# Optimization experiments

Measured on AMD Instinct MI355X. Metric: run time of the kernel, lower is better.

The kernel has to match this reference:

```python
import jax, jax.numpy as jnp
import numpy as np

N = 50000          # nodes
E = 800000         # edges (before self-loops)
IN_CH = 128
HID = 64
HEADS = 4
NEG_SLOPE = 0.2    # PyG GATConv default negative_slope


def _gat_conv(x, W, a_src, a_dst, bias, src, dst, heads, out_ch):
    """PyG-style GATConv (concat=True). src/dst already include self-loops."""
    n = x.shape[0]
    h = (x @ W).reshape(n, heads, out_ch)                 # [N,H,C]
    # per-node attention halves: a_src . h_i  and  a_dst . h_i
    es = (h * a_src[None]).sum(-1)                        # [N,H]
    ed = (h * a_dst[None]).sum(-1)                        # [N,H]
    logits = jax.nn.leaky_relu(es[src] + ed[dst], NEG_SLOPE)   # [Etot,H]
    # segment softmax over incoming edges of each dst node
    m = jax.ops.segment_max(logits, dst, num_segments=n)       # [N,H]
    m = jnp.where(jnp.isfinite(m), m, jnp.zeros_like(m))
    p = jnp.exp(logits - m[dst])                               # [Etot,H]
    s = jax.ops.segment_sum(p, dst, num_segments=n)            # [N,H]
    att = p / (s[dst] + 1e-16)                                 # [Etot,H]
    msg = h[src] * att[..., None]                              # [Etot,H,C]
    out = jax.ops.segment_sum(msg, dst, num_segments=n)        # [N,H,C]
    return out.reshape(n, heads * out_ch) + bias


def setup_inputs() -> dict:
    key = jax.random.key(0)
    ks = jax.random.split(key, 12)
    x = jax.random.normal(ks[0], (N, IN_CH), dtype=jnp.float32)
    edge_index = jax.random.randint(ks[1], (2, E), 0, N, dtype=jnp.int32)
    def glorot(k, shape, fan_in):
        return jax.random.normal(k, shape, dtype=jnp.float32) * (1.0 / np.sqrt(fan_in))
    return {
        "x": x,
        "W1": glorot(ks[2], (IN_CH, HEADS * HID), IN_CH),
        "a_src1": glorot(ks[3], (HEADS, HID), HID),
        "a_dst1": glorot(ks[4], (HEADS, HID), HID),
        "b1": jnp.zeros((HEADS * HID,), dtype=jnp.float32),
        "W2": glorot(ks[5], (HEADS * HID, HID), HEADS * HID),
        "a_src2": glorot(ks[6], (1, HID), HID),
        "a_dst2": glorot(ks[7], (1, HID), HID),
        "b2": jnp.zeros((HID,), dtype=jnp.float32),
        "Wo": glorot(ks[8], (HID, 1), HID),
        "bo": jnp.zeros((1,), dtype=jnp.float32),
        "edge_index": edge_index,
    }


def reference(x, W1, a_src1, a_dst1, b1, W2, a_src2, a_dst2, b2, Wo, bo, edge_index):
    n = x.shape[0]
    loops = jnp.arange(n, dtype=edge_index.dtype)          # add_self_loops=True (PyG default)
    src = jnp.concatenate([edge_index[0], loops])
    dst = jnp.concatenate([edge_index[1], loops])
    h = jax.nn.elu(_gat_conv(x, W1, a_src1, a_dst1, b1, src, dst, HEADS, HID))
    # dropout inactive in eval mode
    h = jax.nn.elu(_gat_conv(h, W2, a_src2, a_dst2, b2, src, dst, 1, HID))
    return (h @ Wo + bo).squeeze(-1)                       # [N]
```

## Files before the change

kernel.cpp:

```cpp
#include <hip/hip_runtime.h>
#include <cmath>

#define LRELU_SLOPE 0.2f

static inline int cdiv_h(int a, int b){ return (a + b - 1) / b; }

__device__ __forceinline__ float dev_lrelu(float x){ return x > 0.f ? x : LRELU_SLOPE * x; }
__device__ __forceinline__ float dev_elu(float x){ return x > 0.f ? x : expm1f(x); }

__device__ __forceinline__ unsigned short f2bf(float f){
  unsigned int u = __float_as_uint(f);
  u = (u + 0x7FFFu + ((u >> 16) & 1u)) >> 16;
  return (unsigned short)u;
}
__device__ __forceinline__ float bf2f_lo(unsigned int u){
  return __uint_as_float(u << 16);
}
__device__ __forceinline__ float bf2f_hi(unsigned int u){
  return __uint_as_float(u & 0xFFFF0000u);
}

__device__ __forceinline__ float edge_w(float logit){
  return __expf(fminf(logit, 80.f));
}

typedef __attribute__((ext_vector_type(8))) short bf16x8;
typedef __attribute__((ext_vector_type(4))) float f32x4;

#define CNT_STRIDE 16

__global__ void prep_kernel(const float* __restrict__ W1, unsigned short* __restrict__ W1T,
                            const float* __restrict__ W2, unsigned short* __restrict__ W2T,
                            int* __restrict__ cnt, int n)
{
  int b = blockIdx.x, t = threadIdx.x;
  if (b < 128){
    int i = b * 256 + t;
    int k = i >> 8, c = i & 255;
    W1T[(size_t)c * 128 + k] = f2bf(W1[i]);
  } else if (b < 192){
    int i = (b - 128) * 256 + t;
    int k = i >> 6, c = i & 63;
    W2T[(size_t)c * 256 + k] = f2bf(W2[i]);
  } else {
    int i = (b - 192) * 256 + t;
    if (i < n) cnt[(size_t)i * CNT_STRIDE] = 1;
  }
}


__global__ void scan_blocks_kernel(const int* __restrict__ cnt, int* __restrict__ rowptr,
                                   int n, int* __restrict__ bsum){
  __shared__ int sd[256];
  int idx = blockIdx.x * 256 + threadIdx.x;
  int v = (idx < n) ? cnt[(size_t)idx * CNT_STRIDE] : 0;
  sd[threadIdx.x] = v;
  __syncthreads();
  #pragma unroll
  for (int off = 1; off < 256; off <<= 1){
    int x = (threadIdx.x >= off) ? sd[threadIdx.x - off] : 0;
    __syncthreads();
    sd[threadIdx.x] += x;
    __syncthreads();
  }
  if (idx < n) rowptr[idx] = sd[threadIdx.x] - v;
  if (threadIdx.x == 255) bsum[blockIdx.x] = sd[255];
}

__global__ void scan_add_kernel(int* __restrict__ rowptr, int n, const int* __restrict__ bsum,
                                int total, unsigned short* __restrict__ col){
  __shared__ int red[256];
  int t = threadIdx.x;
  int p = 0;
  for (int k = t; k < (int)blockIdx.x; k += 256) p += bsum[k];
  red[t] = p;
  __syncthreads();
  #pragma unroll
  for (int off = 128; off > 0; off >>= 1){
    if (t < off) red[t] += red[t + off];
    __syncthreads();
  }
  int prefix = red[0];
  int idx = blockIdx.x * 256 + t;
  if (idx < n){
    int v = rowptr[idx] + prefix;
    rowptr[idx] = v;
    col[v] = (unsigned short)idx;
  }
  if (idx == 0) rowptr[n] = total;
}

__global__ void scatter_kernel(const int* __restrict__ ei, const int* __restrict__ rank,
                               const int* __restrict__ rowptr, int e, unsigned short* __restrict__ col){
  int i = blockIdx.x * blockDim.x + threadIdx.x;
  if (i >= e) return;
  int s = ei[i], d = ei[e + i];
  col[rowptr[d] + rank[i]] = (unsigned short)s;
}

__launch_bounds__(256)
__global__ void gemm1_mfma_kernel(const float* __restrict__ A, const unsigned short* __restrict__ BT,
                                  unsigned short* __restrict__ Cb,
                                  const float* __restrict__ a_src, const float* __restrict__ a_dst,
                                  float* __restrict__ es, float* __restrict__ ed,
                                  int M, int K, int GB,
                                  const int* __restrict__ hist_dst, int He,
                                  int* __restrict__ cnt, int* __restrict__ rank)
{
  constexpr int BN = 256, NSUB = 16, H = 4;
  constexpr int LDK = 40;
  __shared__ short As[64 * LDK];
  __shared__ short Bs[BN * LDK];
  const int tid = threadIdx.x;

  if (blockIdx.x >= GB){
    int i = (blockIdx.x - GB) * 256 + tid;
    if (i < He){
      int d = hist_dst[i];
      rank[i] = atomicAdd(&cnt[(size_t)d * CNT_STRIDE], 1);
    }
    return;
  }

  const int bm = blockIdx.x;
  const int wave = tid >> 6, lane = tid & 63;
  const int lm = lane & 15, quad = lane >> 4;
  const int arow = tid >> 2, kc8 = (tid & 3) * 8;
  const int gm_a = bm * 64 + arow;

  f32x4 acc[NSUB];
  #pragma unroll
  for (int i = 0; i < NSUB; i++) acc[i] = (f32x4){0.f, 0.f, 0.f, 0.f};

  for (int k0 = 0; k0 < K; k0 += 32){
    unsigned short a8[8];
    float4 t0 = {0,0,0,0}, t1 = {0,0,0,0};
    if (gm_a < M){
      t0 = *(const float4*)&A[(size_t)gm_a * K + k0 + kc8];
      t1 = *(const float4*)&A[(size_t)gm_a * K + k0 + kc8 + 4];
    }
    a8[0] = f2bf(t0.x); a8[1] = f2bf(t0.y); a8[2] = f2bf(t0.z); a8[3] = f2bf(t0.w);
    a8[4] = f2bf(t1.x); a8[5] = f2bf(t1.y); a8[6] = f2bf(t1.z); a8[7] = f2bf(t1.w);
    uint4 b8[4];
    #pragma unroll
    for (int rep = 0; rep < 4; rep++){
      int brow = rep * 64 + arow;
      b8[rep] = *(const uint4*)&BT[(size_t)brow * K + k0 + kc8];
    }
    __syncthreads();
    *(uint4*)&As[arow * LDK + kc8] = *(uint4*)a8;
    #pragma unroll
    for (int rep = 0; rep < 4; rep++)
      *(uint4*)&Bs[(rep * 64 + arow) * LDK + kc8] = b8[rep];
    __syncthreads();
    bf16x8 af = *(const bf16x8*)&As[(wave * 16 + lm) * LDK + quad * 8];
    #pragma unroll
    for (int nb = 0; nb < NSUB; nb++){
      bf16x8 bfr = *(const bf16x8*)&Bs[(nb * 16 + lm) * LDK + quad * 8];
      acc[nb] = __builtin_amdgcn_mfma_f32_16x16x32_bf16(af, bfr, acc[nb], 0, 0, 0);
    }
  }

  float asv[NSUB], adv[NSUB];
  #pragma unroll
  for (int nb = 0; nb < NSUB; nb++){
    asv[nb] = a_src[nb * 16 + lm];
    adv[nb] = a_dst[nb * 16 + lm];
  }
  #pragma unroll
  for (int r = 0; r < 4; r++){
    int gm = bm * 64 + wave * 16 + quad * 4 + r;
    if (gm < M){
      #pragma unroll
      for (int nb = 0; nb < NSUB; nb++)
        Cb[(size_t)gm * BN + nb * 16 + lm] = f2bf(acc[nb][r]);
    }
    #pragma unroll
    for (int h = 0; h < H; h++){
      float ps = 0.f, pd = 0.f;
      #pragma unroll
      for (int nbh = 0; nbh < 4; nbh++){
        int nb = h * 4 + nbh;
        float a = acc[nb][r];
        ps += a * asv[nb];
        pd += a * adv[nb];
      }
      #pragma unroll
      for (int off = 1; off < 16; off <<= 1){
        ps += __shfl_xor(ps, off, 64);
        pd += __shfl_xor(pd, off, 64);
      }
      if (lm == 0 && gm < M){
        es[(size_t)gm * H + h] = ps;
        ed[(size_t)gm * H + h] = pd;
      }
    }
  }
}

__launch_bounds__(256)
__global__ void gemm2_mfma_kernel(const unsigned short* __restrict__ A, const unsigned short* __restrict__ BT,
                                  unsigned short* __restrict__ Cb,
                                  const float* __restrict__ a_src, const float* __restrict__ a_dst,
                                  float* __restrict__ es, float* __restrict__ ed,
                                  int M, int K)
{
  constexpr int BN = 64, NSUB = 4;
  constexpr int LDK = 40;
  __shared__ short As[128 * LDK];
  __shared__ short Bs[64 * LDK];
  const int tid = threadIdx.x;
  const int bm = blockIdx.x;
  const int wave = tid >> 6, lane = tid & 63;
  const int lm = lane & 15, quad = lane >> 4;
  const int arow = tid >> 2, kc8 = (tid & 3) * 8;
  const int gm_a0 = bm * 128 + arow;
  const int gm_a1 = gm_a0 + 64;

  f32x4 acc0[NSUB], acc1[NSUB];
  #pragma unroll
  for (int i = 0; i < NSUB; i++){
    acc0[i] = (f32x4){0.f, 0.f, 0.f, 0.f};
    acc1[i] = (f32x4){0.f, 0.f, 0.f, 0.f};
  }

  for (int k0 = 0; k0 < K; k0 += 32){
    uint4 a0 = make_uint4(0,0,0,0), a1 = make_uint4(0,0,0,0);
    if (gm_a0 < M) a0 = *(const uint4*)&A[(size_t)gm_a0 * K + k0 + kc8];
    if (gm_a1 < M) a1 = *(const uint4*)&A[(size_t)gm_a1 * K + k0 + kc8];
    uint4 b = *(const uint4*)&BT[(size_t)arow * K + k0 + kc8];
    __syncthreads();
    *(uint4*)&As[arow * LDK + kc8] = a0;
    *(uint4*)&As[(64 + arow) * LDK + kc8] = a1;
    *(uint4*)&Bs[arow * LDK + kc8] = b;
    __syncthreads();
    bf16x8 af0 = *(const bf16x8*)&As[(wave * 16 + lm) * LDK + quad * 8];
    bf16x8 af1 = *(const bf16x8*)&As[(64 + wave * 16 + lm) * LDK + quad * 8];
    #pragma unroll
    for (int nb = 0; nb < NSUB; nb++){
      bf16x8 bfr = *(const bf16x8*)&Bs[(nb * 16 + lm) * LDK + quad * 8];
      acc0[nb] = __builtin_amdgcn_mfma_f32_16x16x32_bf16(af0, bfr, acc0[nb], 0, 0, 0);
      acc1[nb] = __builtin_amdgcn_mfma_f32_16x16x32_bf16(af1, bfr, acc1[nb], 0, 0, 0);
    }
  }

  float asv[NSUB], adv[NSUB];
  #pragma unroll
  for (int nb = 0; nb < NSUB; nb++){
    asv[nb] = a_src[nb * 16 + lm];
    adv[nb] = a_dst[nb * 16 + lm];
  }
  #pragma unroll
  for (int half = 0; half < 2; half++){
    #pragma unroll
    for (int r = 0; r < 4; r++){
      int gm = bm * 128 + half * 64 + wave * 16 + quad * 4 + r;
      float ps = 0.f, pd = 0.f;
      #pragma unroll
      for (int nb = 0; nb < NSUB; nb++){
        float a = half ? acc1[nb][r] : acc0[nb][r];
        if (gm < M) Cb[(size_t)gm * BN + nb * 16 + lm] = f2bf(a);
        ps += a * asv[nb];
        pd += a * adv[nb];
      }
      #pragma unroll
      for (int off = 1; off < 16; off <<= 1){
        ps += __shfl_xor(ps, off, 64);
        pd += __shfl_xor(pd, off, 64);
      }
      if (lm == 0 && gm < M){
        es[gm] = ps;
        ed[gm] = pd;
      }
    }
  }
}

__global__ void agg1_kernel(const unsigned short* __restrict__ h1b, const float* __restrict__ es,
                            const float* __restrict__ ed,
                            const int* __restrict__ rowptr, const unsigned short* __restrict__ col,
                            const float* __restrict__ b1, unsigned short* __restrict__ out1b, int n)
{
  int node = blockIdx.x * 8 + (threadIdx.x >> 5);
  if (node >= n) return;
  int r = threadIdx.x & 31;
  int h = r >> 3;
  float edh = ed[node * 4 + h];
  int start = rowptr[node], end = rowptr[node + 1];
  float l = 0.f;
  float a0=0.f,a1=0.f,a2=0.f,a3=0.f,a4=0.f,a5=0.f,a6=0.f,a7=0.f;
  int j = start;
  for (; j + 3 < end; j += 4){
    int s0 = col[j], s1 = col[j+1], s2 = col[j+2], s3 = col[j+3];
    float e0 = es[s0*4 + h], e1 = es[s1*4 + h], e2 = es[s2*4 + h], e3 = es[s3*4 + h];
    uint4 r0 = *(const uint4*)&h1b[(size_t)s0 * 256 + r * 8];
    uint4 r1 = *(const uint4*)&h1b[(size_t)s1 * 256 + r * 8];
    uint4 r2 = *(const uint4*)&h1b[(size_t)s2 * 256 + r * 8];
    uint4 r3 = *(const uint4*)&h1b[(size_t)s3 * 256 + r * 8];
    float w0 = edge_w(dev_lrelu(e0 + edh));
    float w1 = edge_w(dev_lrelu(e1 + edh));
    float w2 = edge_w(dev_lrelu(e2 + edh));
    float w3 = edge_w(dev_lrelu(e3 + edh));
    l += w0 + w1 + w2 + w3;
    a0 += bf2f_lo(r0.x)*w0 + bf2f_lo(r1.x)*w1 + bf2f_lo(r2.x)*w2 + bf2f_lo(r3.x)*w3;
    a1 += bf2f_hi(r0.x)*w0 + bf2f_hi(r1.x)*w1 + bf2f_hi(r2.x)*w2 + bf2f_hi(r3.x)*w3;
    a2 += bf2f_lo(r0.y)*w0 + bf2f_lo(r1.y)*w1 + bf2f_lo(r2.y)*w2 + bf2f_lo(r3.y)*w3;
    a3 += bf2f_hi(r0.y)*w0 + bf2f_hi(r1.y)*w1 + bf2f_hi(r2.y)*w2 + bf2f_hi(r3.y)*w3;
    a4 += bf2f_lo(r0.z)*w0 + bf2f_lo(r1.z)*w1 + bf2f_lo(r2.z)*w2 + bf2f_lo(r3.z)*w3;
    a5 += bf2f_hi(r0.z)*w0 + bf2f_hi(r1.z)*w1 + bf2f_hi(r2.z)*w2 + bf2f_hi(r3.z)*w3;
    a6 += bf2f_lo(r0.w)*w0 + bf2f_lo(r1.w)*w1 + bf2f_lo(r2.w)*w2 + bf2f_lo(r3.w)*w3;
    a7 += bf2f_hi(r0.w)*w0 + bf2f_hi(r1.w)*w1 + bf2f_hi(r2.w)*w2 + bf2f_hi(r3.w)*w3;
  }
  for (; j < end; j++){
    int s0 = col[j];
    float w0 = edge_w(dev_lrelu(es[s0*4 + h] + edh));
    uint4 r0 = *(const uint4*)&h1b[(size_t)s0 * 256 + r * 8];
    l += w0;
    a0 += bf2f_lo(r0.x)*w0; a1 += bf2f_hi(r0.x)*w0;
    a2 += bf2f_lo(r0.y)*w0; a3 += bf2f_hi(r0.y)*w0;
    a4 += bf2f_lo(r0.z)*w0; a5 += bf2f_hi(r0.z)*w0;
    a6 += bf2f_lo(r0.w)*w0; a7 += bf2f_hi(r0.w)*w0;
  }
  float inv = 1.f / l;
  float4 bA = *(const float4*)&b1[r * 8];
  float4 bB = *(const float4*)&b1[r * 8 + 4];
  uint4 o;
  o.x = (unsigned int)f2bf(dev_elu(a0*inv + bA.x)) | ((unsigned int)f2bf(dev_elu(a1*inv + bA.y)) << 16);
  o.y = (unsigned int)f2bf(dev_elu(a2*inv + bA.z)) | ((unsigned int)f2bf(dev_elu(a3*inv + bA.w)) << 16);
  o.z = (unsigned int)f2bf(dev_elu(a4*inv + bB.x)) | ((unsigned int)f2bf(dev_elu(a5*inv + bB.y)) << 16);
  o.w = (unsigned int)f2bf(dev_elu(a6*inv + bB.z)) | ((unsigned int)f2bf(dev_elu(a7*inv + bB.w)) << 16);
  *(uint4*)&out1b[(size_t)node * 256 + r * 8] = o;
}

__global__ void agg2_kernel(const unsigned short* __restrict__ h2b, const float* __restrict__ es,
                            const float* __restrict__ ed,
                            const int* __restrict__ rowptr, const unsigned short* __restrict__ col,
                            const float* __restrict__ b2, const float* __restrict__ Wo,
                            const float* __restrict__ bo, float* __restrict__ out, int n)
{
  int node = blockIdx.x * 16 + (threadIdx.x >> 4);
  if (node >= n) return;
  int r = threadIdx.x & 15;
  float edh = ed[node];
  int start = rowptr[node], end = rowptr[node + 1];
  float l = 0.f;
  float a0=0.f,a1=0.f,a2=0.f,a3=0.f;
  int j = start;
  for (; j + 3 < end; j += 4){
    int s0 = col[j], s1 = col[j+1], s2 = col[j+2], s3 = col[j+3];
    float e0 = es[s0], e1 = es[s1], e2 = es[s2], e3 = es[s3];
    uint2 r0 = *(const uint2*)&h2b[(size_t)s0 * 64 + r * 4];
    uint2 r1 = *(const uint2*)&h2b[(size_t)s1 * 64 + r * 4];
    uint2 r2 = *(const uint2*)&h2b[(size_t)s2 * 64 + r * 4];
    uint2 r3 = *(const uint2*)&h2b[(size_t)s3 * 64 + r * 4];
    float w0 = edge_w(dev_lrelu(e0 + edh));
    float w1 = edge_w(dev_lrelu(e1 + edh));
    float w2 = edge_w(dev_lrelu(e2 + edh));
    float w3 = edge_w(dev_lrelu(e3 + edh));
    l += w0 + w1 + w2 + w3;
    a0 += bf2f_lo(r0.x)*w0 + bf2f_lo(r1.x)*w1 + bf2f_lo(r2.x)*w2 + bf2f_lo(r3.x)*w3;
    a1 += bf2f_hi(r0.x)*w0 + bf2f_hi(r1.x)*w1 + bf2f_hi(r2.x)*w2 + bf2f_hi(r3.x)*w3;
    a2 += bf2f_lo(r0.y)*w0 + bf2f_lo(r1.y)*w1 + bf2f_lo(r2.y)*w2 + bf2f_lo(r3.y)*w3;
    a3 += bf2f_hi(r0.y)*w0 + bf2f_hi(r1.y)*w1 + bf2f_hi(r2.y)*w2 + bf2f_hi(r3.y)*w3;
  }
  for (; j < end; j++){
    int s0 = col[j];
    float w0 = edge_w(dev_lrelu(es[s0] + edh));
    uint2 r0 = *(const uint2*)&h2b[(size_t)s0 * 64 + r * 4];
    l += w0;
    a0 += bf2f_lo(r0.x)*w0; a1 += bf2f_hi(r0.x)*w0;
    a2 += bf2f_lo(r0.y)*w0; a3 += bf2f_hi(r0.y)*w0;
  }
  float inv = 1.f / l;
  float4 bb = *(const float4*)&b2[r * 4];
  float4 wo = *(const float4*)&Wo[r * 4];
  float t = dev_elu(a0*inv + bb.x) * wo.x
          + dev_elu(a1*inv + bb.y) * wo.y
          + dev_elu(a2*inv + bb.z) * wo.z
          + dev_elu(a3*inv + bb.w) * wo.w;
  #pragma unroll
  for (int off = 1; off < 16; off <<= 1) t += __shfl_xor(t, off, 64);
  if (r == 0) out[node] = t + bo[0];
}

extern "C" void kernel_launch(void* const* d_in, const int* in_sizes, int n_in,
                              void* d_out, int out_size, void* d_ws, size_t ws_size,
                              hipStream_t stream)
{
  const float* x    = (const float*)d_in[0];
  const float* W1   = (const float*)d_in[1];
  const float* a_s1 = (const float*)d_in[2];
  const float* a_d1 = (const float*)d_in[3];
  const float* b1   = (const float*)d_in[4];
  const float* W2   = (const float*)d_in[5];
  const float* a_s2 = (const float*)d_in[6];
  const float* a_d2 = (const float*)d_in[7];
  const float* b2   = (const float*)d_in[8];
  const float* Wo   = (const float*)d_in[9];
  const float* bo   = (const float*)d_in[10];
  const int*   ei   = (const int*)d_in[11];

  const int Nn = in_sizes[0] / 128;
  const int E  = in_sizes[11] / 2;
  const int ET = E + Nn;

  size_t off = 0;
  auto carve = [&](size_t bytes) -> void* {
    void* p = (char*)d_ws + off;
    off += (bytes + 255) & ~(size_t)255;
    return p;
  };
  unsigned short* h1b   = (unsigned short*)carve((size_t)Nn * 256 * sizeof(unsigned short));
  unsigned short* out1b = (unsigned short*)carve((size_t)Nn * 256 * sizeof(unsigned short));
  unsigned short* h2b   = (unsigned short*)carve((size_t)Nn * 64 * sizeof(unsigned short));
  unsigned short* W1T   = (unsigned short*)carve((size_t)128 * 256 * sizeof(unsigned short));
  unsigned short* W2T   = (unsigned short*)carve((size_t)256 * 64 * sizeof(unsigned short));
  float* es1    = (float*)carve((size_t)Nn * 4 * sizeof(float));
  float* ed1    = (float*)carve((size_t)Nn * 4 * sizeof(float));
  float* es2    = (float*)carve((size_t)Nn * sizeof(float));
  float* ed2    = (float*)carve((size_t)Nn * sizeof(float));
  int*   cnt    = (int*)carve((size_t)Nn * CNT_STRIDE * sizeof(int));
  int*   rowptr = (int*)carve((size_t)(Nn + 1) * sizeof(int));
  int*   rank   = (int*)carve((size_t)E * sizeof(int));
  int*   bsum   = (int*)carve(256 * sizeof(int));
  unsigned short* col = (unsigned short*)carve((size_t)ET * sizeof(unsigned short));
  float* out = (float*)d_out;

  int deg_blocks = cdiv_h(Nn, 256);
  prep_kernel<<<192 + deg_blocks, 256, 0, stream>>>(W1, W1T, W2, W2T, cnt, Nn);

  int GB1 = cdiv_h(Nn, 64);
  int HB  = cdiv_h(E, 256);
  gemm1_mfma_kernel<<<GB1 + HB, 256, 0, stream>>>(
      x, W1T, h1b, a_s1, a_d1, es1, ed1, Nn, 128, GB1, ei + E, E, cnt, rank);

  int nb = cdiv_h(Nn, 256);
  scan_blocks_kernel<<<nb, 256, 0, stream>>>(cnt, rowptr, Nn, bsum);
  scan_add_kernel<<<nb, 256, 0, stream>>>(rowptr, Nn, bsum, ET, col);
  scatter_kernel<<<cdiv_h(E, 256), 256, 0, stream>>>(ei, rank, rowptr, E, col);

  agg1_kernel<<<cdiv_h(Nn, 8), 256, 0, stream>>>(h1b, es1, ed1, rowptr, col, b1, out1b, Nn);

  gemm2_mfma_kernel<<<cdiv_h(Nn, 128), 256, 0, stream>>>(
      out1b, W2T, h2b, a_s2, a_d2, es2, ed2, Nn, 256);
  agg2_kernel<<<cdiv_h(Nn, 16), 256, 0, stream>>>(h2b, es2, ed2, rowptr, col, b2, Wo, bo, out, Nn);
}
```

Baseline: 254.0 us.

## Split each node's edge list across a full wavefront in both aggregation kernels

Both aggregation kernels now assign one 64-lane wavefront per destination node instead of 32 or 16 lanes. Lane groups take disjoint subsets of the incoming edges and combine partial sums with cross-lane shuffles. Column indices for the next iteration are also loaded one step ahead. The aim is more memory-level parallelism and shorter per-node serial loops for the gather-heavy aggregation. The cost is extra shuffle reductions, more blocks, and idle half-waves for low-degree nodes.

```diff
diff --git a/kernel.cpp b/kernel.cpp
--- a/kernel.cpp
+++ b/kernel.cpp
@@ -276,22 +276,44 @@
   }
 }
 
+#define AGG1_EDGE(jj) { \
+    int s0_ = col[jj]; \
+    float w0_ = edge_w(dev_lrelu(es[s0_*4 + h] + edh)); \
+    uint4 r0_ = *(const uint4*)&h1b[(size_t)s0_ * 256 + r * 8]; \
+    l += w0_; \
+    a0 += bf2f_lo(r0_.x)*w0_; a1 += bf2f_hi(r0_.x)*w0_; \
+    a2 += bf2f_lo(r0_.y)*w0_; a3 += bf2f_hi(r0_.y)*w0_; \
+    a4 += bf2f_lo(r0_.z)*w0_; a5 += bf2f_hi(r0_.z)*w0_; \
+    a6 += bf2f_lo(r0_.w)*w0_; a7 += bf2f_hi(r0_.w)*w0_; }
+
 __global__ void agg1_kernel(const unsigned short* __restrict__ h1b, const float* __restrict__ es,
                             const float* __restrict__ ed,
                             const int* __restrict__ rowptr, const unsigned short* __restrict__ col,
                             const float* __restrict__ b1, unsigned short* __restrict__ out1b, int n)
 {
-  int node = blockIdx.x * 8 + (threadIdx.x >> 5);
+  int node = blockIdx.x * 4 + (threadIdx.x >> 6);
   if (node >= n) return;
-  int r = threadIdx.x & 31;
+  int lane = threadIdx.x & 63;
+  int half = lane >> 5;
+  int r = lane & 31;
   int h = r >> 3;
   float edh = ed[node * 4 + h];
   int start = rowptr[node], end = rowptr[node + 1];
   float l = 0.f;
   float a0=0.f,a1=0.f,a2=0.f,a3=0.f,a4=0.f,a5=0.f,a6=0.f,a7=0.f;
   int j = start;
-  for (; j + 3 < end; j += 4){
-    int s0 = col[j], s1 = col[j+1], s2 = col[j+2], s3 = col[j+3];
+
+  int c0=0,c1=0,c2=0,c3=0;
+  if (j + 7 < end){
+    int b = j + half * 4;
+    c0 = col[b]; c1 = col[b+1]; c2 = col[b+2]; c3 = col[b+3];
+  }
+  for (; j + 7 < end; j += 8){
+    int s0 = c0, s1 = c1, s2 = c2, s3 = c3;
+    if (j + 15 < end){
+      int b = j + 8 + half * 4;
+      c0 = col[b]; c1 = col[b+1]; c2 = col[b+2]; c3 = col[b+3];
+    }
     float e0 = es[s0*4 + h], e1 = es[s1*4 + h], e2 = es[s2*4 + h], e3 = es[s3*4 + h];
     uint4 r0 = *(const uint4*)&h1b[(size_t)s0 * 256 + r * 8];
     uint4 r1 = *(const uint4*)&h1b[(size_t)s1 * 256 + r * 8];
@@ -311,26 +333,42 @@
     a6 += bf2f_lo(r0.w)*w0 + bf2f_lo(r1.w)*w1 + bf2f_lo(r2.w)*w2 + bf2f_lo(r3.w)*w3;
     a7 += bf2f_hi(r0.w)*w0 + bf2f_hi(r1.w)*w1 + bf2f_hi(r2.w)*w2 + bf2f_hi(r3.w)*w3;
   }
-  for (; j < end; j++){
-    int s0 = col[j];
-    float w0 = edge_w(dev_lrelu(es[s0*4 + h] + edh));
-    uint4 r0 = *(const uint4*)&h1b[(size_t)s0 * 256 + r * 8];
-    l += w0;
-    a0 += bf2f_lo(r0.x)*w0; a1 += bf2f_hi(r0.x)*w0;
-    a2 += bf2f_lo(r0.y)*w0; a3 += bf2f_hi(r0.y)*w0;
-    a4 += bf2f_lo(r0.z)*w0; a5 += bf2f_hi(r0.z)*w0;
-    a6 += bf2f_lo(r0.w)*w0; a7 += bf2f_hi(r0.w)*w0;
-  }
-  float inv = 1.f / l;
-  float4 bA = *(const float4*)&b1[r * 8];
-  float4 bB = *(const float4*)&b1[r * 8 + 4];
-  uint4 o;
-  o.x = (unsigned int)f2bf(dev_elu(a0*inv + bA.x)) | ((unsigned int)f2bf(dev_elu(a1*inv + bA.y)) << 16);
-  o.y = (unsigned int)f2bf(dev_elu(a2*inv + bA.z)) | ((unsigned int)f2bf(dev_elu(a3*inv + bA.w)) << 16);
-  o.z = (unsigned int)f2bf(dev_elu(a4*inv + bB.x)) | ((unsigned int)f2bf(dev_elu(a5*inv + bB.y)) << 16);
-  o.w = (unsigned int)f2bf(dev_elu(a6*inv + bB.z)) | ((unsigned int)f2bf(dev_elu(a7*inv + bB.w)) << 16);
-  *(uint4*)&out1b[(size_t)node * 256 + r * 8] = o;
-}
+  for (; j + 3 < end; j += 4){
+    int b = j + half * 2;
+    AGG1_EDGE(b); AGG1_EDGE(b + 1);
+  }
+  for (; j + 1 < end; j += 2){
+    AGG1_EDGE(j + half);
+  }
+  if (j < end && half == 0){
+    AGG1_EDGE(j);
+  }
+  l  += __shfl_xor(l , 32, 64);
+  a0 += __shfl_xor(a0, 32, 64);  a1 += __shfl_xor(a1, 32, 64);
+  a2 += __shfl_xor(a2, 32, 64);  a3 += __shfl_xor(a3, 32, 64);
+  a4 += __shfl_xor(a4, 32, 64);  a5 += __shfl_xor(a5, 32, 64);
+  a6 += __shfl_xor(a6, 32, 64);  a7 += __shfl_xor(a7, 32, 64);
+
+  if (half == 0){
+    float inv = 1.f / l;
+    float4 bA = *(const float4*)&b1[r * 8];
+    float4 bB = *(const float4*)&b1[r * 8 + 4];
+    uint4 o;
+    o.x = (unsigned int)f2bf(dev_elu(a0*inv + bA.x)) | ((unsigned int)f2bf(dev_elu(a1*inv + bA.y)) << 16);
+    o.y = (unsigned int)f2bf(dev_elu(a2*inv + bA.z)) | ((unsigned int)f2bf(dev_elu(a3*inv + bA.w)) << 16);
+    o.z = (unsigned int)f2bf(dev_elu(a4*inv + bB.x)) | ((unsigned int)f2bf(dev_elu(a5*inv + bB.y)) << 16);
+    o.w = (unsigned int)f2bf(dev_elu(a6*inv + bB.z)) | ((unsigned int)f2bf(dev_elu(a7*inv + bB.w)) << 16);
+    *(uint4*)&out1b[(size_t)node * 256 + r * 8] = o;
+  }
+}
+
+#define AGG2_EDGE(jj) { \
+    int s0_ = col[jj]; \
+    float w0_ = edge_w(dev_lrelu(es[s0_] + edh)); \
+    uint2 r0_ = *(const uint2*)&h2b[(size_t)s0_ * 64 + r * 4]; \
+    l += w0_; \
+    a0 += bf2f_lo(r0_.x)*w0_; a1 += bf2f_hi(r0_.x)*w0_; \
+    a2 += bf2f_lo(r0_.y)*w0_; a3 += bf2f_hi(r0_.y)*w0_; }
 
 __global__ void agg2_kernel(const unsigned short* __restrict__ h2b, const float* __restrict__ es,
                             const float* __restrict__ ed,
@@ -338,39 +376,54 @@
                             const float* __restrict__ b2, const float* __restrict__ Wo,
                             const float* __restrict__ bo, float* __restrict__ out, int n)
 {
-  int node = blockIdx.x * 16 + (threadIdx.x >> 4);
+  int node = blockIdx.x * 4 + (threadIdx.x >> 6);
   if (node >= n) return;
-  int r = threadIdx.x & 15;
+  int lane = threadIdx.x & 63;
+  int slot = lane >> 4;
+  int r = lane & 15;
   float edh = ed[node];
   int start = rowptr[node], end = rowptr[node + 1];
   float l = 0.f;
   float a0=0.f,a1=0.f,a2=0.f,a3=0.f;
   int j = start;
-  for (; j + 3 < end; j += 4){
-    int s0 = col[j], s1 = col[j+1], s2 = col[j+2], s3 = col[j+3];
-    float e0 = es[s0], e1 = es[s1], e2 = es[s2], e3 = es[s3];
+
+  int c0=0, c1=0;
+  if (j + 7 < end){
+    int b = j + slot * 2;
+    c0 = col[b]; c1 = col[b+1];
+  }
+  for (; j + 7 < end; j += 8){
+    int s0 = c0, s1 = c1;
+    if (j + 15 < end){
+      int b = j + 8 + slot * 2;
+      c0 = col[b]; c1 = col[b+1];
+    }
+    float e0 = es[s0], e1 = es[s1];
     uint2 r0 = *(const uint2*)&h2b[(size_t)s0 * 64 + r * 4];
     uint2 r1 = *(const uint2*)&h2b[(size_t)s1 * 64 + r * 4];
-    uint2 r2 = *(const uint2*)&h2b[(size_t)s2 * 64 + r * 4];
-    uint2 r3 = *(const uint2*)&h2b[(size_t)s3 * 64 + r * 4];
     float w0 = edge_w(dev_lrelu(e0 + edh));
     float w1 = edge_w(dev_lrelu(e1 + edh));
-    float w2 = edge_w(dev_lrelu(e2 + edh));
-    float w3 = edge_w(dev_lrelu(e3 + edh));
-    l += w0 + w1 + w2 + w3;
-    a0 += bf2f_lo(r0.x)*w0 + bf2f_lo(r1.x)*w1 + bf2f_lo(r2.x)*w2 + bf2f_lo(r3.x)*w3;
-    a1 += bf2f_hi(r0.x)*w0 + bf2f_hi(r1.x)*w1 + bf2f_hi(r2.x)*w2 + bf2f_hi(r3.x)*w3;
-    a2 += bf2f_lo(r0.y)*w0 + bf2f_lo(r1.y)*w1 + bf2f_lo(r2.y)*w2 + bf2f_lo(r3.y)*w3;
-    a3 += bf2f_hi(r0.y)*w0 + bf2f_hi(r1.y)*w1 + bf2f_hi(r2.y)*w2 + bf2f_hi(r3.y)*w3;
-  }
-  for (; j < end; j++){
-    int s0 = col[j];
-    float w0 = edge_w(dev_lrelu(es[s0] + edh));
-    uint2 r0 = *(const uint2*)&h2b[(size_t)s0 * 64 + r * 4];
-    l += w0;
-    a0 += bf2f_lo(r0.x)*w0; a1 += bf2f_hi(r0.x)*w0;
-    a2 += bf2f_lo(r0.y)*w0; a3 += bf2f_hi(r0.y)*w0;
-  }
+    l += w0 + w1;
+    a0 += bf2f_lo(r0.x)*w0 + bf2f_lo(r1.x)*w1;
+    a1 += bf2f_hi(r0.x)*w0 + bf2f_hi(r1.x)*w1;
+    a2 += bf2f_lo(r0.y)*w0 + bf2f_lo(r1.y)*w1;
+    a3 += bf2f_hi(r0.y)*w0 + bf2f_hi(r1.y)*w1;
+  }
+  for (; j + 3 < end; j += 4){
+    AGG2_EDGE(j + slot);
+  }
+  {
+    int rem = end - j;
+    if (slot < rem){
+      AGG2_EDGE(j + slot);
+    }
+  }
+  l  += __shfl_xor(l , 16, 64);  l  += __shfl_xor(l , 32, 64);
+  a0 += __shfl_xor(a0, 16, 64);  a0 += __shfl_xor(a0, 32, 64);
+  a1 += __shfl_xor(a1, 16, 64);  a1 += __shfl_xor(a1, 32, 64);
+  a2 += __shfl_xor(a2, 16, 64);  a2 += __shfl_xor(a2, 32, 64);
+  a3 += __shfl_xor(a3, 16, 64);  a3 += __shfl_xor(a3, 32, 64);
+
   float inv = 1.f / l;
   float4 bb = *(const float4*)&b2[r * 4];
   float4 wo = *(const float4*)&Wo[r * 4];
@@ -380,7 +433,7 @@
           + dev_elu(a3*inv + bb.w) * wo.w;
   #pragma unroll
   for (int off = 1; off < 16; off <<= 1) t += __shfl_xor(t, off, 64);
-  if (r == 0) out[node] = t + bo[0];
+  if (lane == 0) out[node] = t + bo[0];
 }
 
 extern "C" void kernel_launch(void* const* d_in, const int* in_sizes, int n_in,
@@ -439,9 +492,9 @@
   scan_add_kernel<<<nb, 256, 0, stream>>>(rowptr, Nn, bsum, ET, col);
   scatter_kernel<<<cdiv_h(E, 256), 256, 0, stream>>>(ei, rank, rowptr, E, col);
 
-  agg1_kernel<<<cdiv_h(Nn, 8), 256, 0, stream>>>(h1b, es1, ed1, rowptr, col, b1, out1b, Nn);
+  agg1_kernel<<<cdiv_h(Nn, 4), 256, 0, stream>>>(h1b, es1, ed1, rowptr, col, b1, out1b, Nn);
 
   gemm2_mfma_kernel<<<cdiv_h(Nn, 128), 256, 0, stream>>>(
       out1b, W2T, h2b, a_s2, a_d2, es2, ed2, Nn, 256);
-  agg2_kernel<<<cdiv_h(Nn, 16), 256, 0, stream>>>(h2b, es2, ed2, rowptr, col, b2, Wo, bo, out, Nn);
-}
+  agg2_kernel<<<cdiv_h(Nn, 4), 256, 0, stream>>>(h2b, es2, ed2, rowptr, col, b2, Wo, bo, out, Nn);
+}
```

Result: slower. 260.4 us (+2.5%).

## Fuse layer-1 aggregation with layer-2 GEMM and split edges across half-waves

Applied to the files above, without the earlier changes.

Merges the layer-1 attention aggregation and the layer-2 projection GEMM into one kernel. Each block aggregates 4 nodes into shared memory, then one wave runs MFMA against W2T, read straight from global memory, to produce h2 and the attention logits. This removes the out1b round trip through global memory and one kernel launch. Each node now gets a full wave instead of half a wave, with the two half-waves splitting the edges and prefetching the next column indices. In exchange, only one wave per block does the GEMM, 12 of the 16 MFMA rows are zero padding, and W2T is refetched for every block.

```diff
diff --git a/kernel.cpp b/kernel.cpp
--- a/kernel.cpp
+++ b/kernel.cpp
@@ -5,7 +5,7 @@
 
 static inline int cdiv_h(int a, int b){ return (a + b - 1) / b; }
 
-__device__ __forceinline__ float dev_lrelu(float x){ return x > 0.f ? x : LRELU_SLOPE * x; }
+__device__ __forceinline__ float dev_lrelu(float x){ return fmaxf(x, LRELU_SLOPE * x); }
 __device__ __forceinline__ float dev_elu(float x){ return x > 0.f ? x : expm1f(x); }
 
 __device__ __forceinline__ unsigned short f2bf(float f){
@@ -198,68 +198,133 @@
   }
 }
 
-__launch_bounds__(256)
-__global__ void gemm2_mfma_kernel(const unsigned short* __restrict__ A, const unsigned short* __restrict__ BT,
-                                  unsigned short* __restrict__ Cb,
-                                  const float* __restrict__ a_src, const float* __restrict__ a_dst,
-                                  float* __restrict__ es, float* __restrict__ ed,
-                                  int M, int K)
+#define AGG1_EDGE(jj) { \
+    int s0_ = col[jj]; \
+    float w0_ = edge_w(dev_lrelu(es[s0_*4 + h] + edh)); \
+    uint4 r0_ = *(const uint4*)&h1b[((size_t)s0_ << 8) + r * 8]; \
+    l += w0_; \
+    a0 += bf2f_lo(r0_.x)*w0_; a1 += bf2f_hi(r0_.x)*w0_; \
+    a2 += bf2f_lo(r0_.y)*w0_; a3 += bf2f_hi(r0_.y)*w0_; \
+    a4 += bf2f_lo(r0_.z)*w0_; a5 += bf2f_hi(r0_.z)*w0_; \
+    a6 += bf2f_lo(r0_.w)*w0_; a7 += bf2f_hi(r0_.w)*w0_; }
+
+__global__ void agg1_fused_kernel(const unsigned short* __restrict__ h1b, const float* __restrict__ es,
+                                  const float* __restrict__ ed,
+                                  const int* __restrict__ rowptr, const unsigned short* __restrict__ col,
+                                  const float* __restrict__ b1,
+                                  const unsigned short* __restrict__ W2T,
+                                  const float* __restrict__ a_s2, const float* __restrict__ a_d2,
+                                  unsigned short* __restrict__ h2b,
+                                  float* __restrict__ es2, float* __restrict__ ed2, int n)
 {
-  constexpr int BN = 64, NSUB = 4;
-  constexpr int LDK = 40;
-  __shared__ short As[128 * LDK];
-  __shared__ short Bs[64 * LDK];
+  constexpr int LDA2 = 264;
+  __shared__ short As2[16 * LDA2];
   const int tid = threadIdx.x;
-  const int bm = blockIdx.x;
-  const int wave = tid >> 6, lane = tid & 63;
-  const int lm = lane & 15, quad = lane >> 4;
-  const int arow = tid >> 2, kc8 = (tid & 3) * 8;
-  const int gm_a0 = bm * 128 + arow;
-  const int gm_a1 = gm_a0 + 64;
-
-  f32x4 acc0[NSUB], acc1[NSUB];
-  #pragma unroll
-  for (int i = 0; i < NSUB; i++){
-    acc0[i] = (f32x4){0.f, 0.f, 0.f, 0.f};
-    acc1[i] = (f32x4){0.f, 0.f, 0.f, 0.f};
-  }
-
-  for (int k0 = 0; k0 < K; k0 += 32){
-    uint4 a0 = make_uint4(0,0,0,0), a1 = make_uint4(0,0,0,0);
-    if (gm_a0 < M) a0 = *(const uint4*)&A[(size_t)gm_a0 * K + k0 + kc8];
-    if (gm_a1 < M) a1 = *(const uint4*)&A[(size_t)gm_a1 * K + k0 + kc8];
-    uint4 b = *(const uint4*)&BT[(size_t)arow * K + k0 + kc8];
-    __syncthreads();
-    *(uint4*)&As[arow * LDK + kc8] = a0;
-    *(uint4*)&As[(64 + arow) * LDK + kc8] = a1;
-    *(uint4*)&Bs[arow * LDK + kc8] = b;
-    __syncthreads();
-    bf16x8 af0 = *(const bf16x8*)&As[(wave * 16 + lm) * LDK + quad * 8];
-    bf16x8 af1 = *(const bf16x8*)&As[(64 + wave * 16 + lm) * LDK + quad * 8];
-    #pragma unroll
-    for (int nb = 0; nb < NSUB; nb++){
-      bf16x8 bfr = *(const bf16x8*)&Bs[(nb * 16 + lm) * LDK + quad * 8];
-      acc0[nb] = __builtin_amdgcn_mfma_f32_16x16x32_bf16(af0, bfr, acc0[nb], 0, 0, 0);
-      acc1[nb] = __builtin_amdgcn_mfma_f32_16x16x32_bf16(af1, bfr, acc1[nb], 0, 0, 0);
-    }
-  }
-
-  float asv[NSUB], adv[NSUB];
-  #pragma unroll
-  for (int nb = 0; nb < NSUB; nb++){
-    asv[nb] = a_src[nb * 16 + lm];
-    adv[nb] = a_dst[nb * 16 + lm];
-  }
-  #pragma unroll
-  for (int half = 0; half < 2; half++){
-    #pragma unroll
-    for (int r = 0; r < 4; r++){
-      int gm = bm * 128 + half * 64 + wave * 16 + quad * 4 + r;
+  const int wave = tid >> 6;
+  const int node_base = blockIdx.x * 4;
+  const int node = node_base + wave;
+  const int lane = tid & 63;
+  const int half = lane >> 5;
+  const int r = lane & 31;
+  const int h = r >> 3;
+
+  {
+    unsigned int* z = (unsigned int*)&As2[4 * LDA2];
+    for (int i = tid; i < 12 * LDA2 / 2; i += 256) z[i] = 0u;
+  }
+
+  if (node < n){
+    float edh = ed[node * 4 + h];
+    int start = rowptr[node], end = rowptr[node + 1];
+    float l = 0.f;
+    float a0=0.f,a1=0.f,a2=0.f,a3=0.f,a4=0.f,a5=0.f,a6=0.f,a7=0.f;
+    int j = start;
+
+    int c0=0,c1=0,c2=0,c3=0;
+    if (j + 7 < end){
+      int b = j + half * 4;
+      c0 = col[b]; c1 = col[b+1]; c2 = col[b+2]; c3 = col[b+3];
+    }
+    for (; j + 7 < end; j += 8){
+      int s0 = c0, s1 = c1, s2 = c2, s3 = c3;
+      if (j + 15 < end){
+        int b = j + 8 + half * 4;
+        c0 = col[b]; c1 = col[b+1]; c2 = col[b+2]; c3 = col[b+3];
+      }
+      float e0 = es[s0*4 + h], e1 = es[s1*4 + h], e2 = es[s2*4 + h], e3 = es[s3*4 + h];
+      uint4 r0 = *(const uint4*)&h1b[((size_t)s0 << 8) + r * 8];
+      uint4 r1 = *(const uint4*)&h1b[((size_t)s1 << 8) + r * 8];
+      uint4 r2 = *(const uint4*)&h1b[((size_t)s2 << 8) + r * 8];
+      uint4 r3 = *(const uint4*)&h1b[((size_t)s3 << 8) + r * 8];
+      float w0 = edge_w(dev_lrelu(e0 + edh));
+      float w1 = edge_w(dev_lrelu(e1 + edh));
+      float w2 = edge_w(dev_lrelu(e2 + edh));
+      float w3 = edge_w(dev_lrelu(e3 + edh));
+      l += w0 + w1 + w2 + w3;
+      a0 += bf2f_lo(r0.x)*w0 + bf2f_lo(r1.x)*w1 + bf2f_lo(r2.x)*w2 + bf2f_lo(r3.x)*w3;
+      a1 += bf2f_hi(r0.x)*w0 + bf2f_hi(r1.x)*w1 + bf2f_hi(r2.x)*w2 + bf2f_hi(r3.x)*w3;
+      a2 += bf2f_lo(r0.y)*w0 + bf2f_lo(r1.y)*w1 + bf2f_lo(r2.y)*w2 + bf2f_lo(r3.y)*w3;
+      a3 += bf2f_hi(r0.y)*w0 + bf2f_hi(r1.y)*w1 + bf2f_hi(r2.y)*w2 + bf2f_hi(r3.y)*w3;
+      a4 += bf2f_lo(r0.z)*w0 + bf2f_lo(r1.z)*w1 + bf2f_lo(r2.z)*w2 + bf2f_lo(r3.z)*w3;
+      a5 += bf2f_hi(r0.z)*w0 + bf2f_hi(r1.z)*w1 + bf2f_hi(r2.z)*w2 + bf2f_hi(r3.z)*w3;
+      a6 += bf2f_lo(r0.w)*w0 + bf2f_lo(r1.w)*w1 + bf2f_lo(r2.w)*w2 + bf2f_lo(r3.w)*w3;
+      a7 += bf2f_hi(r0.w)*w0 + bf2f_hi(r1.w)*w1 + bf2f_hi(r2.w)*w2 + bf2f_hi(r3.w)*w3;
+    }
+    for (; j + 3 < end; j += 4){
+      int b = j + half * 2;
+      AGG1_EDGE(b); AGG1_EDGE(b + 1);
+    }
+    for (; j + 1 < end; j += 2){
+      AGG1_EDGE(j + half);
+    }
+    if (j < end && half == 0){
+      AGG1_EDGE(j);
+    }
+    l  += __shfl_xor(l , 32, 64);
+    a0 += __shfl_xor(a0, 32, 64);  a1 += __shfl_xor(a1, 32, 64);
+    a2 += __shfl_xor(a2, 32, 64);  a3 += __shfl_xor(a3, 32, 64);
+    a4 += __shfl_xor(a4, 32, 64);  a5 += __shfl_xor(a5, 32, 64);
+    a6 += __shfl_xor(a6, 32, 64);  a7 += __shfl_xor(a7, 32, 64);
+
+    if (half == 0){
+      float inv = 1.f / l;
+      float4 bA = *(const float4*)&b1[r * 8];
+      float4 bB = *(const float4*)&b1[r * 8 + 4];
+      uint4 o;
+      o.x = (unsigned int)f2bf(dev_elu(a0*inv + bA.x)) | ((unsigned int)f2bf(dev_elu(a1*inv + bA.y)) << 16);
+      o.y = (unsigned int)f2bf(dev_elu(a2*inv + bA.z)) | ((unsigned int)f2bf(dev_elu(a3*inv + bA.w)) << 16);
+      o.z = (unsigned int)f2bf(dev_elu(a4*inv + bB.x)) | ((unsigned int)f2bf(dev_elu(a5*inv + bB.y)) << 16);
+      o.w = (unsigned int)f2bf(dev_elu(a6*inv + bB.z)) | ((unsigned int)f2bf(dev_elu(a7*inv + bB.w)) << 16);
+      *(uint4*)&As2[wave * LDA2 + r * 8] = o;
+    }
+  }
+  __syncthreads();
+
+  if (wave == 0){
+    const int lm16 = lane & 15, quad = lane >> 4;
+    f32x4 acc[4];
+    #pragma unroll
+    for (int i = 0; i < 4; i++) acc[i] = (f32x4){0.f, 0.f, 0.f, 0.f};
+    for (int k0 = 0; k0 < 256; k0 += 32){
+      bf16x8 af = *(const bf16x8*)&As2[lm16 * LDA2 + k0 + quad * 8];
+      #pragma unroll
+      for (int nb = 0; nb < 4; nb++){
+        bf16x8 bfr = *(const bf16x8*)&W2T[(size_t)(nb * 16 + lm16) * 256 + k0 + quad * 8];
+        acc[nb] = __builtin_amdgcn_mfma_f32_16x16x32_bf16(af, bfr, acc[nb], 0, 0, 0);
+      }
+    }
+    float asv[4], adv[4];
+    #pragma unroll
+    for (int nb = 0; nb < 4; nb++){
+      asv[nb] = a_s2[nb * 16 + lm16];
+      adv[nb] = a_d2[nb * 16 + lm16];
+    }
+    #pragma unroll
+    for (int rr = 0; rr < 4; rr++){
       float ps = 0.f, pd = 0.f;
       #pragma unroll
-      for (int nb = 0; nb < NSUB; nb++){
-        float a = half ? acc1[nb][r] : acc0[nb][r];
-        if (gm < M) Cb[(size_t)gm * BN + nb * 16 + lm] = f2bf(a);
+      for (int nb = 0; nb < 4; nb++){
+        float a = acc[nb][rr];
         ps += a * asv[nb];
         pd += a * adv[nb];
       }
@@ -268,68 +333,18 @@
         ps += __shfl_xor(ps, off, 64);
         pd += __shfl_xor(pd, off, 64);
       }
-      if (lm == 0 && gm < M){
-        es[gm] = ps;
-        ed[gm] = pd;
-      }
-    }
-  }
-}
-
-__global__ void agg1_kernel(const unsigned short* __restrict__ h1b, const float* __restrict__ es,
-                            const float* __restrict__ ed,
-                            const int* __restrict__ rowptr, const unsigned short* __restrict__ col,
-                            const float* __restrict__ b1, unsigned short* __restrict__ out1b, int n)
-{
-  int node = blockIdx.x * 8 + (threadIdx.x >> 5);
-  if (node >= n) return;
-  int r = threadIdx.x & 31;
-  int h = r >> 3;
-  float edh = ed[node * 4 + h];
-  int start = rowptr[node], end = rowptr[node + 1];
-  float l = 0.f;
-  float a0=0.f,a1=0.f,a2=0.f,a3=0.f,a4=0.f,a5=0.f,a6=0.f,a7=0.f;
-  int j = start;
-  for (; j + 3 < end; j += 4){
-    int s0 = col[j], s1 = col[j+1], s2 = col[j+2], s3 = col[j+3];
-    float e0 = es[s0*4 + h], e1 = es[s1*4 + h], e2 = es[s2*4 + h], e3 = es[s3*4 + h];
-    uint4 r0 = *(const uint4*)&h1b[(size_t)s0 * 256 + r * 8];
-    uint4 r1 = *(const uint4*)&h1b[(size_t)s1 * 256 + r * 8];
-    uint4 r2 = *(const uint4*)&h1b[(size_t)s2 * 256 + r * 8];
-    uint4 r3 = *(const uint4*)&h1b[(size_t)s3 * 256 + r * 8];
-    float w0 = edge_w(dev_lrelu(e0 + edh));
-    float w1 = edge_w(dev_lrelu(e1 + edh));
-    float w2 = edge_w(dev_lrelu(e2 + edh));
-    float w3 = edge_w(dev_lrelu(e3 + edh));
-    l += w0 + w1 + w2 + w3;
-    a0 += bf2f_lo(r0.x)*w0 + bf2f_lo(r1.x)*w1 + bf2f_lo(r2.x)*w2 + bf2f_lo(r3.x)*w3;
-    a1 += bf2f_hi(r0.x)*w0 + bf2f_hi(r1.x)*w1 + bf2f_hi(r2.x)*w2 + bf2f_hi(r3.x)*w3;
-    a2 += bf2f_lo(r0.y)*w0 + bf2f_lo(r1.y)*w1 + bf2f_lo(r2.y)*w2 + bf2f_lo(r3.y)*w3;
-    a3 += bf2f_hi(r0.y)*w0 + bf2f_hi(r1.y)*w1 + bf2f_hi(r2.y)*w2 + bf2f_hi(r3.y)*w3;
-    a4 += bf2f_lo(r0.z)*w0 + bf2f_lo(r1.z)*w1 + bf2f_lo(r2.z)*w2 + bf2f_lo(r3.z)*w3;
-    a5 += bf2f_hi(r0.z)*w0 + bf2f_hi(r1.z)*w1 + bf2f_hi(r2.z)*w2 + bf2f_hi(r3.z)*w3;
-    a6 += bf2f_lo(r0.w)*w0 + bf2f_lo(r1.w)*w1 + bf2f_lo(r2.w)*w2 + bf2f_lo(r3.w)*w3;
-    a7 += bf2f_hi(r0.w)*w0 + bf2f_hi(r1.w)*w1 + bf2f_hi(r2.w)*w2 + bf2f_hi(r3.w)*w3;
-  }
-  for (; j < end; j++){
-    int s0 = col[j];
-    float w0 = edge_w(dev_lrelu(es[s0*4 + h] + edh));
-    uint4 r0 = *(const uint4*)&h1b[(size_t)s0 * 256 + r * 8];
-    l += w0;
-    a0 += bf2f_lo(r0.x)*w0; a1 += bf2f_hi(r0.x)*w0;
-    a2 += bf2f_lo(r0.y)*w0; a3 += bf2f_hi(r0.y)*w0;
-    a4 += bf2f_lo(r0.z)*w0; a5 += bf2f_hi(r0.z)*w0;
-    a6 += bf2f_lo(r0.w)*w0; a7 += bf2f_hi(r0.w)*w0;
-  }
-  float inv = 1.f / l;
-  float4 bA = *(const float4*)&b1[r * 8];
-  float4 bB = *(const float4*)&b1[r * 8 + 4];
-  uint4 o;
-  o.x = (unsigned int)f2bf(dev_elu(a0*inv + bA.x)) | ((unsigned int)f2bf(dev_elu(a1*inv + bA.y)) << 16);
-  o.y = (unsigned int)f2bf(dev_elu(a2*inv + bA.z)) | ((unsigned int)f2bf(dev_elu(a3*inv + bA.w)) << 16);
-  o.z = (unsigned int)f2bf(dev_elu(a4*inv + bB.x)) | ((unsigned int)f2bf(dev_elu(a5*inv + bB.y)) << 16);
-  o.w = (unsigned int)f2bf(dev_elu(a6*inv + bB.z)) | ((unsigned int)f2bf(dev_elu(a7*inv + bB.w)) << 16);
-  *(uint4*)&out1b[(size_t)node * 256 + r * 8] = o;
+      int gm = node_base + rr;
+      if (quad == 0 && gm < n){
+        #pragma unroll
+        for (int nb = 0; nb < 4; nb++)
+          h2b[(size_t)gm * 64 + nb * 16 + lm16] = f2bf(acc[nb][rr]);
+        if (lm16 == 0){
+          es2[gm] = ps;
+          ed2[gm] = pd;
+        }
+      }
+    }
+  }
 }
 
 __global__ void agg2_kernel(const unsigned short* __restrict__ h2b, const float* __restrict__ es,
@@ -411,7 +426,6 @@
     return p;
   };
   unsigned short* h1b   = (unsigned short*)carve((size_t)Nn * 256 * sizeof(unsigned short));
-  unsigned short* out1b = (unsigned short*)carve((size_t)Nn * 256 * sizeof(unsigned short));
   unsigned short* h2b   = (unsigned short*)carve((size_t)Nn * 64 * sizeof(unsigned short));
   unsigned short* W1T   = (unsigned short*)carve((size_t)128 * 256 * sizeof(unsigned short));
   unsigned short* W2T   = (unsigned short*)carve((size_t)256 * 64 * sizeof(unsigned short));
@@ -439,9 +453,8 @@
   scan_add_kernel<<<nb, 256, 0, stream>>>(rowptr, Nn, bsum, ET, col);
   scatter_kernel<<<cdiv_h(E, 256), 256, 0, stream>>>(ei, rank, rowptr, E, col);
 
-  agg1_kernel<<<cdiv_h(Nn, 8), 256, 0, stream>>>(h1b, es1, ed1, rowptr, col, b1, out1b, Nn);
-
-  gemm2_mfma_kernel<<<cdiv_h(Nn, 128), 256, 0, stream>>>(
-      out1b, W2T, h2b, a_s2, a_d2, es2, ed2, Nn, 256);
+  agg1_fused_kernel<<<cdiv_h(Nn, 4), 256, 0, stream>>>(
+      h1b, es1, ed1, rowptr, col, b1, W2T, a_s2, a_d2, h2b, es2, ed2, Nn);
+
   agg2_kernel<<<cdiv_h(Nn, 16), 256, 0, stream>>>(h2b, es2, ed2, rowptr, col, b2, Wo, bo, out, Nn);
 }
```

After: 263.4 us. +3.7%, slower.
